# Performance work log

Measured on AMD Instinct MI355X. Metric: run time of the kernel, lower is better.

The kernel has to match this reference:

```python
import jax, jax.numpy as jnp
import numpy as np

EPS = 1e-6

def setup_inputs() -> dict:
    key = jax.random.key(0)
    N, E, d_i, d_o = 2048, 65536, 128, 128
    k = jax.random.split(key, 8)
    x = jax.random.normal(k[0], (N, d_i), dtype=jnp.float32)
    src = jax.random.randint(k[1], (E,), 0, N)
    tgt = jax.random.randint(k[2], (E,), 0, N)
    adj = jnp.zeros((N, N), dtype=jnp.float32)  # unused by forward math
    # incidence matrices: Msrc[n,e]=1 iff src[e]==n, Mtgt[n,e]=1 iff tgt[e]==n
    Msrc = jax.nn.one_hot(src, N, dtype=jnp.float32).T  # [N,E]
    Mtgt = jax.nn.one_hot(tgt, N, dtype=jnp.float32).T  # [N,E]
    # xavier-uniform linear weights, stored as [in, out]
    lim_f = float(np.sqrt(6.0 / (2 * d_i + d_o)))
    lim_w = float(np.sqrt(6.0 / (2 * d_i + 1)))
    fW = jax.random.uniform(k[3], (2 * d_i, d_o), minval=-lim_f, maxval=lim_f, dtype=jnp.float32)
    fb = jax.random.normal(k[4], (d_o,), dtype=jnp.float32) * 0.01
    wW = jax.random.uniform(k[5], (2 * d_i, 1), minval=-lim_w, maxval=lim_w, dtype=jnp.float32)
    wb = jax.random.normal(k[6], (1,), dtype=jnp.float32) * 0.01
    return {"x": x, "adj": adj, "src": src, "tgt": tgt, "Msrc": Msrc,
            "Mtgt": Mtgt, "fW": fW, "fb": fb, "wW": wW, "wb": wb}

def reference(x, adj, src, tgt, Msrc, Mtgt, fW, fb, wW, wb):
    # gather endpoint features per edge and concatenate: [E, 2*d_i]
    h = jnp.concatenate([x[src], x[tgt]], axis=1)
    y = jax.nn.relu(h @ fW + fb)          # [E, d_o] edge messages
    a = h @ wW + wb                        # [E, 1] attention logits
    a_exp = jnp.exp(a - jnp.max(a, axis=0, keepdims=True))  # global-max-stabilized exp
    a_sum = Mtgt @ a_exp + EPS             # [N, 1] per-target softmax denominator
    o = (Mtgt @ (y * a_exp)) / a_sum       # [N, d_o] attention-weighted aggregation
    return o
```

## Files before the change

### kernel.cpp

```cpp
#include <hip/hip_runtime.h>
#include <math.h>

#define NN 2048
#define D  128
#define EE 65536
#define EPSF 1e-6f

__global__ void k0_init(int* __restrict__ counts, unsigned int* __restrict__ amax_bits) {
    int i = blockIdx.x * blockDim.x + threadIdx.x;
    if (i < NN) counts[i] = 0;
    if (i == 0) *amax_bits = 0xFF800000u;
}

__global__ __launch_bounds__(128) void k1_node_proj(
        const float* __restrict__ x, const float* __restrict__ fW,
        const float* __restrict__ wW,
        float* __restrict__ U, float* __restrict__ V,
        float* __restrict__ p, float* __restrict__ q) {
    int n = blockIdx.x;
    int t = threadIdx.x;
    __shared__ float xs[D];
    xs[t] = x[n * D + t];
    __syncthreads();
    float u = 0.f, v = 0.f;
#pragma unroll 8
    for (int k = 0; k < D; ++k) {
        float xv = xs[k];
        u = fmaf(xv, fW[k * D + t], u);
        v = fmaf(xv, fW[(k + D) * D + t], v);
    }
    U[n * D + t] = u;
    V[n * D + t] = v;

    float pp = xs[t] * wW[t];
    float qq = xs[t] * wW[D + t];
#pragma unroll
    for (int off = 32; off > 0; off >>= 1) {
        pp += __shfl_down(pp, off, 64);
        qq += __shfl_down(qq, off, 64);
    }
    __shared__ float red[4];
    int wave = t >> 6;
    if ((t & 63) == 0) { red[wave * 2] = pp; red[wave * 2 + 1] = qq; }
    __syncthreads();
    if (t == 0) {
        p[n] = red[0] + red[2];
        q[n] = red[1] + red[3];
    }
}

__global__ __launch_bounds__(256) void k2_logit_max_count(
        const int* __restrict__ src, const int* __restrict__ tgt,
        const float* __restrict__ p, const float* __restrict__ q,
        const float* __restrict__ wb,
        float* __restrict__ a, unsigned int* __restrict__ amax_bits,
        int* __restrict__ counts) {
    int i = blockIdx.x * blockDim.x + threadIdx.x;
    float local = -INFINITY;
    float wbv = wb[0];
    for (int e = i; e < EE; e += gridDim.x * blockDim.x) {
        int t = tgt[e];
        float ae = p[src[e]] + q[t] + wbv;
        a[e] = ae;
        local = fmaxf(local, ae);
        atomicAdd(&counts[t], 1);
    }
#pragma unroll
    for (int off = 32; off > 0; off >>= 1)
        local = fmaxf(local, __shfl_down(local, off, 64));
    __shared__ float smax[4];
    if ((threadIdx.x & 63) == 0) smax[threadIdx.x >> 6] = local;
    __syncthreads();
    if (threadIdx.x == 0) {
        float m = fmaxf(fmaxf(smax[0], smax[1]), fmaxf(smax[2], smax[3]));
        if (m >= 0.f) atomicMax((int*)amax_bits, __float_as_int(m));
        else          atomicMin(amax_bits, __float_as_uint(m));
    }
}

__global__ __launch_bounds__(256) void k_scan(const int* __restrict__ counts,
                                              int* __restrict__ rowptr,
                                              int* __restrict__ cursor) {
    __shared__ int sums[256];
    int t = threadIdx.x;
    int base = t * 8;
    int local[8];
    int s = 0;
#pragma unroll
    for (int i = 0; i < 8; ++i) { local[i] = s; s += counts[base + i]; }
    sums[t] = s;
    __syncthreads();
    for (int off = 1; off < 256; off <<= 1) {
        int v = sums[t];
        int add = (t >= off) ? sums[t - off] : 0;
        __syncthreads();
        sums[t] = v + add;
        __syncthreads();
    }
    int prefix = (t > 0) ? sums[t - 1] : 0;
#pragma unroll
    for (int i = 0; i < 8; ++i) {
        int rp = prefix + local[i];
        rowptr[base + i] = rp;
        cursor[base + i] = rp;
    }
    if (t == 255) rowptr[NN] = sums[255];
}

__global__ __launch_bounds__(256) void k_fill(const int* __restrict__ tgt,
                                              int* __restrict__ cursor,
                                              int* __restrict__ elist) {
    int e = blockIdx.x * blockDim.x + threadIdx.x;
    if (e < EE) {
        int pos = atomicAdd(&cursor[tgt[e]], 1);
        elist[pos] = e;
    }
}

__global__ __launch_bounds__(128) void k_agg(
        const int* __restrict__ rowptr, const int* __restrict__ elist,
        const int* __restrict__ src, const float* __restrict__ a,
        const unsigned int* __restrict__ amax_bits,
        const float* __restrict__ U, const float* __restrict__ V,
        const float* __restrict__ fb, float* __restrict__ o) {
    int n = blockIdx.x;
    int c = threadIdx.x;
    float amax = __uint_as_float(*amax_bits);
    float vn = V[n * D + c] + fb[c];
    float acc = 0.f, den = 0.f;
    int jb = rowptr[n], je = rowptr[n + 1];
    for (int j = jb; j < je; ++j) {
        int e = elist[j];
        float aexp = expf(a[e] - amax);
        int s = src[e];
        float yv = fmaxf(U[s * D + c] + vn, 0.f);
        acc = fmaf(yv, aexp, acc);
        den += aexp;
    }
    o[n * D + c] = acc / (den + EPSF);
}

extern "C" void kernel_launch(void* const* d_in, const int* in_sizes, int n_in,
                              void* d_out, int out_size, void* d_ws, size_t ws_size,
                              hipStream_t stream) {
    const float* x   = (const float*)d_in[0];
    const int*   src = (const int*)d_in[2];
    const int*   tgt = (const int*)d_in[3];
    const float* fW  = (const float*)d_in[6];
    const float* fb  = (const float*)d_in[7];
    const float* wW  = (const float*)d_in[8];
    const float* wb  = (const float*)d_in[9];
    float* o = (float*)d_out;

    float* ws = (float*)d_ws;
    float* U     = ws;
    float* V     = U + NN * D;
    float* p     = V + NN * D;
    float* q     = p + NN;
    float* a     = q + NN;
    unsigned int* amax_bits = (unsigned int*)(a + EE);
    int* counts = (int*)(amax_bits + 8);
    int* rowptr = counts + NN;
    int* cursor = rowptr + NN + 8;
    int* elist  = cursor + NN;

    k0_init<<<(NN + 255) / 256, 256, 0, stream>>>(counts, amax_bits);
    k1_node_proj<<<NN, 128, 0, stream>>>(x, fW, wW, U, V, p, q);
    k2_logit_max_count<<<EE / 256, 256, 0, stream>>>(src, tgt, p, q, wb, a,
                                                     amax_bits, counts);
    k_scan<<<1, 256, 0, stream>>>(counts, rowptr, cursor);
    k_fill<<<EE / 256, 256, 0, stream>>>(tgt, cursor, elist);
    k_agg<<<NN, 128, 0, stream>>>(rowptr, elist, src, a, amax_bits, U, V, fb, o);
}
```

Before: 837.2 us.

## Fuse logit computation into aggregation with per-target softmax max

Removes the separate logit/global-max kernel and init kernel, moving edge counting into the node projection kernel and using memset for zeroing. The aggregation kernel now computes edge logits from p/q, takes a per-target max, and caches source ids and exp weights in shared memory before the feature accumulation loop. This trims launches, global atomics and per-edge dependent loads; the per-target max slightly changes how EPS scales relative to the reference.

After: 823.0 us. About the same (-1.7%).

```diff
diff --git a/kernel.cpp b/kernel.cpp
--- a/kernel.cpp
+++ b/kernel.cpp
@@ -4,21 +4,21 @@
 #define NN 2048
 #define D  128
 #define EE 65536
+#define EPB 32
+#define CAP 512
 #define EPSF 1e-6f
 
-__global__ void k0_init(int* __restrict__ counts, unsigned int* __restrict__ amax_bits) {
-    int i = blockIdx.x * blockDim.x + threadIdx.x;
-    if (i < NN) counts[i] = 0;
-    if (i == 0) *amax_bits = 0xFF800000u;
-}
-
-__global__ __launch_bounds__(128) void k1_node_proj(
+__global__ __launch_bounds__(128) void k1_proj_count(
         const float* __restrict__ x, const float* __restrict__ fW,
-        const float* __restrict__ wW,
+        const float* __restrict__ wW, const int* __restrict__ tgt,
         float* __restrict__ U, float* __restrict__ V,
-        float* __restrict__ p, float* __restrict__ q) {
+        float* __restrict__ p, float* __restrict__ q,
+        int* __restrict__ counts) {
     int n = blockIdx.x;
     int t = threadIdx.x;
+
+    if (t < EPB) atomicAdd(&counts[tgt[n * EPB + t]], 1);
+
     __shared__ float xs[D];
     xs[t] = x[n * D + t];
     __syncthreads();
@@ -46,35 +46,6 @@
     if (t == 0) {
         p[n] = red[0] + red[2];
         q[n] = red[1] + red[3];
-    }
-}
-
-__global__ __launch_bounds__(256) void k2_logit_max_count(
-        const int* __restrict__ src, const int* __restrict__ tgt,
-        const float* __restrict__ p, const float* __restrict__ q,
-        const float* __restrict__ wb,
-        float* __restrict__ a, unsigned int* __restrict__ amax_bits,
-        int* __restrict__ counts) {
-    int i = blockIdx.x * blockDim.x + threadIdx.x;
-    float local = -INFINITY;
-    float wbv = wb[0];
-    for (int e = i; e < EE; e += gridDim.x * blockDim.x) {
-        int t = tgt[e];
-        float ae = p[src[e]] + q[t] + wbv;
-        a[e] = ae;
-        local = fmaxf(local, ae);
-        atomicAdd(&counts[t], 1);
-    }
-#pragma unroll
-    for (int off = 32; off > 0; off >>= 1)
-        local = fmaxf(local, __shfl_down(local, off, 64));
-    __shared__ float smax[4];
-    if ((threadIdx.x & 63) == 0) smax[threadIdx.x >> 6] = local;
-    __syncthreads();
-    if (threadIdx.x == 0) {
-        float m = fmaxf(fmaxf(smax[0], smax[1]), fmaxf(smax[2], smax[3]));
-        if (m >= 0.f) atomicMax((int*)amax_bits, __float_as_int(m));
-        else          atomicMin(amax_bits, __float_as_uint(m));
     }
 }
 
@@ -119,25 +90,67 @@
 
 __global__ __launch_bounds__(128) void k_agg(
         const int* __restrict__ rowptr, const int* __restrict__ elist,
-        const int* __restrict__ src, const float* __restrict__ a,
-        const unsigned int* __restrict__ amax_bits,
+        const int* __restrict__ src,
+        const float* __restrict__ p, const float* __restrict__ q,
+        const float* __restrict__ wb,
         const float* __restrict__ U, const float* __restrict__ V,
         const float* __restrict__ fb, float* __restrict__ o) {
     int n = blockIdx.x;
-    int c = threadIdx.x;
-    float amax = __uint_as_float(*amax_bits);
-    float vn = V[n * D + c] + fb[c];
-    float acc = 0.f, den = 0.f;
+    int t = threadIdx.x;
     int jb = rowptr[n], je = rowptr[n + 1];
-    for (int j = jb; j < je; ++j) {
-        int e = elist[j];
-        float aexp = expf(a[e] - amax);
+    int deg = je - jb;
+
+    __shared__ int   s_src[CAP];
+    __shared__ float s_axp[CAP];
+    __shared__ float warpm[2], warpd[2];
+
+    float qn = q[n] + wb[0];
+
+    float lm = -INFINITY;
+    for (int j = t; j < deg; j += 128) {
+        int e = elist[jb + j];
         int s = src[e];
-        float yv = fmaxf(U[s * D + c] + vn, 0.f);
-        acc = fmaf(yv, aexp, acc);
-        den += aexp;
+        float ae = p[s] + qn;
+        if (j < CAP) { s_src[j] = s; s_axp[j] = ae; }
+        lm = fmaxf(lm, ae);
     }
-    o[n * D + c] = acc / (den + EPSF);
+#pragma unroll
+    for (int off = 32; off > 0; off >>= 1)
+        lm = fmaxf(lm, __shfl_down(lm, off, 64));
+    if ((t & 63) == 0) warpm[t >> 6] = lm;
+    __syncthreads();
+    float m = fmaxf(warpm[0], warpm[1]);
+
+    float ld = 0.f;
+    for (int j = t; j < deg; j += 128) {
+        float ax;
+        if (j < CAP) { ax = expf(s_axp[j] - m); s_axp[j] = ax; }
+        else { int e = elist[jb + j]; ax = expf(p[src[e]] + qn - m); }
+        ld += ax;
+    }
+#pragma unroll
+    for (int off = 32; off > 0; off >>= 1)
+        ld += __shfl_down(ld, off, 64);
+    if ((t & 63) == 0) warpd[t >> 6] = ld;
+    __syncthreads();
+    float den = warpd[0] + warpd[1] + EPSF;
+
+    float vn = V[n * D + t] + fb[t];
+    float acc = 0.f;
+    int dc = (deg < CAP) ? deg : CAP;
+#pragma unroll 4
+    for (int j = 0; j < dc; ++j) {
+        int s = s_src[j];
+        float ax = s_axp[j];
+        acc = fmaf(fmaxf(U[s * D + t] + vn, 0.f), ax, acc);
+    }
+    for (int j = CAP; j < deg; ++j) {
+        int e = elist[jb + j];
+        int s = src[e];
+        float ax = expf(p[s] + qn - m);
+        acc = fmaf(fmaxf(U[s * D + t] + vn, 0.f), ax, acc);
+    }
+    o[n * D + t] = acc / den;
 }
 
 extern "C" void kernel_launch(void* const* d_in, const int* in_sizes, int n_in,
@@ -153,22 +166,18 @@
     float* o = (float*)d_out;
 
     float* ws = (float*)d_ws;
-    float* U     = ws;
-    float* V     = U + NN * D;
-    float* p     = V + NN * D;
-    float* q     = p + NN;
-    float* a     = q + NN;
-    unsigned int* amax_bits = (unsigned int*)(a + EE);
-    int* counts = (int*)(amax_bits + 8);
-    int* rowptr = counts + NN;
-    int* cursor = rowptr + NN + 8;
-    int* elist  = cursor + NN;
+    float* U      = ws;
+    float* V      = U + NN * D;
+    float* p      = V + NN * D;
+    float* q      = p + NN;
+    int*   counts = (int*)(q + NN);
+    int*   rowptr = counts + NN;
+    int*   cursor = rowptr + NN + 8;
+    int*   elist  = cursor + NN;
 
-    k0_init<<<(NN + 255) / 256, 256, 0, stream>>>(counts, amax_bits);
-    k1_node_proj<<<NN, 128, 0, stream>>>(x, fW, wW, U, V, p, q);
-    k2_logit_max_count<<<EE / 256, 256, 0, stream>>>(src, tgt, p, q, wb, a,
-                                                     amax_bits, counts);
+    hipMemsetAsync(counts, 0, NN * sizeof(int), stream);
+    k1_proj_count<<<NN, 128, 0, stream>>>(x, fW, wW, tgt, U, V, p, q, counts);
     k_scan<<<1, 256, 0, stream>>>(counts, rowptr, cursor);
     k_fill<<<EE / 256, 256, 0, stream>>>(tgt, cursor, elist);
-    k_agg<<<NN, 128, 0, stream>>>(rowptr, elist, src, a, amax_bits, U, V, fb, o);
+    k_agg<<<NN, 128, 0, stream>>>(rowptr, elist, src, p, q, wb, U, V, fb, o);
 }
```
